# Kernel tuning notes

Measured on AMD Instinct MI355X. Metric: run time of the kernel, lower is better.

Reference implementation:

```python
import jax, jax.numpy as jnp
import numpy as np

INPUT_SIZE = 64
HIDDEN = 128
BATCH = 512
SEQ = 512


def setup_inputs() -> dict:
    key = jax.random.key(0)
    ks = jax.random.split(key, 7)
    s_ih = 1.0 / np.sqrt(HIDDEN)
    token = jax.random.normal(ks[0], (BATCH, SEQ, INPUT_SIZE), dtype=jnp.float32)
    W_ih = jax.random.uniform(ks[1], (HIDDEN, INPUT_SIZE), jnp.float32, -s_ih, s_ih)
    W_hh = jax.random.uniform(ks[2], (HIDDEN, HIDDEN), jnp.float32, -s_ih, s_ih)
    b_ih = jax.random.uniform(ks[3], (HIDDEN,), jnp.float32, -s_ih, s_ih)
    b_hh = jax.random.uniform(ks[4], (HIDDEN,), jnp.float32, -s_ih, s_ih)
    W_lin = jax.random.uniform(ks[5], (1, HIDDEN), jnp.float32, -s_ih, s_ih)
    b_lin = jax.random.uniform(ks[6], (1,), jnp.float32, -s_ih, s_ih)
    return {"token": token, "W_ih": W_ih, "W_hh": W_hh, "b_ih": b_ih,
            "b_hh": b_hh, "W_lin": W_lin, "b_lin": b_lin}


def reference(token, W_ih, W_hh, b_ih, b_hh, W_lin, b_lin):
    # Precompute input projection for all timesteps: [T, B, H]
    x_proj = jnp.einsum('bti,hi->tbh', token, W_ih) + b_ih + b_hh
    h0 = jnp.zeros((token.shape[0], W_hh.shape[0]), dtype=token.dtype)

    def step(h, xp):
        h_new = jnp.tanh(xp + h @ W_hh.T)
        return h_new, None

    h_last, _ = jax.lax.scan(step, h0, x_proj)
    # Linear head on last hidden state: [B, 1]
    return h_last @ W_lin.T + b_lin
```

## Files before the change

### kernel.cpp

```cpp
#include <hip/hip_runtime.h>

#define B_ 512
#define T_ 512
#define I_ 64
#define H_ 128
#define CHUNK 64
#define NCHUNK (T_ / CHUNK)

typedef float4 f4;

__device__ __forceinline__ float fast_tanh(float x) {
    float e = __expf(2.0f * x);
    return 1.0f - 2.0f * __builtin_amdgcn_rcpf(e + 1.0f);
}

template <int CTRL, int BANK>
__device__ __forceinline__ float dppf(float x) {
    return __int_as_float(__builtin_amdgcn_update_dpp(
        0, __float_as_int(x), CTRL, 0xF, BANK, true));
}

__device__ __forceinline__ void gload_lds16(const float* g, float* l) {
    __builtin_amdgcn_global_load_lds(
        (const __attribute__((address_space(1))) unsigned int*)g,
        (__attribute__((address_space(3))) unsigned int*)l, 16, 0, 0);
}

#define FMA4(A, X, W)                      \
    A.x = fmaf((X).x, (W).x, A.x);         \
    A.y = fmaf((X).y, (W).y, A.y);         \
    A.z = fmaf((X).z, (W).z, A.z);         \
    A.w = fmaf((X).w, (W).w, A.w);

#define PIN4(v) asm volatile("" : "+v"((v).x), "+v"((v).y), "+v"((v).z), "+v"((v).w))

__global__ __launch_bounds__(512) __attribute__((amdgpu_waves_per_eu(4, 4)))
void rnn_kernel(const float* __restrict__ token,
                const float* __restrict__ W_ih,
                const float* __restrict__ W_hh,
                const float* __restrict__ b_ih,
                const float* __restrict__ b_hh,
                const float* __restrict__ W_lin,
                const float* __restrict__ b_lin,
                float* __restrict__ out)
{
    __shared__ f4 tok_l[2][CHUNK * 16];
    __shared__ f4 h_l[2][32];

    const int tid = threadIdx.x;
    const int l   = tid & 63;
    const int e   = l & 7;
    const int G   = tid >> 3;
    const int b   = blockIdx.x;

    f4 wh0[4], wh1[4], wi0[2], wi1[2];
    {
        const f4* r0 = (const f4*)(W_hh + (2 * G) * H_ + e * 16);
        const f4* r1 = (const f4*)(W_hh + (2 * G + 1) * H_ + e * 16);
#pragma unroll
        for (int m = 0; m < 4; ++m) { wh0[m] = r0[m]; wh1[m] = r1[m]; }
        const f4* i0 = (const f4*)(W_ih + (2 * G) * I_ + e * 8);
        const f4* i1 = (const f4*)(W_ih + (2 * G + 1) * I_ + e * 8);
#pragma unroll
        for (int m = 0; m < 2; ++m) { wi0[m] = i0[m]; wi1[m] = i1[m]; }
#pragma unroll
        for (int m = 0; m < 4; ++m) { PIN4(wh0[m]); PIN4(wh1[m]); }
        PIN4(wi0[0]); PIN4(wi0[1]); PIN4(wi1[0]); PIN4(wi1[1]);
    }
    const int   jsel    = 2 * G + (e & 1);
    const float my_bias = b_ih[jsel] + b_hh[jsel];
    const int   wloc    = ((jsel >> 2) & 3) * 32 + (jsel >> 4) * 4 + (jsel & 3);
    const bool  writer  = (e < 2);

    const float* tok_row = token + (size_t)b * T_ * I_;

#pragma unroll
    for (int it = 0; it < 2; ++it) {
        const int S = it * 512 + tid;
        const int tt = S >> 4, k = S & 15, m2 = k >> 3, ek = k & 7;
        gload_lds16(tok_row + tt * 64 + ek * 8 + m2 * 4, (float*)&tok_l[0][S]);
    }
    if (tid < H_) ((float*)h_l[0])[tid] = 0.0f;
    asm volatile("s_waitcnt vmcnt(0) lgkmcnt(0)" ::: "memory");
    __builtin_amdgcn_s_barrier();

    f4 t4[2];
    t4[0] = tok_l[0][e];
    t4[1] = tok_l[0][8 + e];

    auto STEP = [&](const f4* hrd, float* hwr, int tt, bool last_in_chunk,
                    bool has_next_chunk, int cb) {
        f4 A0 = {0.f, 0.f, 0.f, 0.f}, A1 = {0.f, 0.f, 0.f, 0.f};
        FMA4(A0, t4[0], wi0[0]);  FMA4(A1, t4[0], wi1[0]);
        FMA4(A0, t4[1], wi0[1]);  FMA4(A1, t4[1], wi1[1]);
#pragma unroll
        for (int m = 0; m < 4; ++m) {
            f4 hv = hrd[m * 8 + e];
            FMA4(A0, hv, wh0[m]);
            FMA4(A1, hv, wh1[m]);
        }
        float p0 = (A0.x + A0.y) + (A0.z + A0.w);
        float p1 = (A1.x + A1.y) + (A1.z + A1.w);
        p0 += dppf<0xB1, 0xF>(p0);
        p1 += dppf<0xB1, 0xF>(p1);
        float c = (e & 1) ? p1 : p0;
        c += dppf<0x4E, 0xF>(c);
        float d1 = dppf<0x104, 0x5>(c);
        float d2 = dppf<0x114, 0xA>(c);
        c = c + d1 + d2;
        float hn = fast_tanh(c + my_bias);
        if (writer) hwr[wloc] = hn;

        if (!last_in_chunk) {
            __builtin_amdgcn_sched_barrier(0);
            t4[0] = tok_l[cb][(tt + 1) * 16 + e];
            t4[1] = tok_l[cb][(tt + 1) * 16 + 8 + e];
            __builtin_amdgcn_sched_barrier(0);
            asm volatile("s_waitcnt lgkmcnt(2)" ::: "memory");
            __builtin_amdgcn_s_barrier();
        } else {
            asm volatile("s_waitcnt vmcnt(0) lgkmcnt(0)" ::: "memory");
            __builtin_amdgcn_s_barrier();
            if (has_next_chunk) {
                t4[0] = tok_l[cb ^ 1][e];
                t4[1] = tok_l[cb ^ 1][8 + e];
            }
        }
    };

#pragma unroll 1
    for (int c = 0; c < NCHUNK; ++c) {
        const int cb = c & 1;
        const bool has_next = (c + 1 < NCHUNK);
        if (has_next) {
            const float* g = tok_row + (size_t)(c + 1) * CHUNK * I_;
#pragma unroll
            for (int it = 0; it < 2; ++it) {
                const int S = it * 512 + tid;
                const int tt = S >> 4, k = S & 15, m2 = k >> 3, ek = k & 7;
                gload_lds16(g + tt * 64 + ek * 8 + m2 * 4, (float*)&tok_l[cb ^ 1][S]);
            }
        }
#pragma unroll 1
        for (int tt = 0; tt < CHUNK; tt += 2) {
            STEP((const f4*)h_l[0], (float*)h_l[1], tt, false, has_next, cb);
            STEP((const f4*)h_l[1], (float*)h_l[0], tt + 1, (tt + 1 == CHUNK - 1),
                 has_next, cb);
        }
    }

    if (tid < 64) {
        const int j0 = tid, j1 = tid + 64;
        const int l0 = ((j0 >> 2) & 3) * 32 + (j0 >> 4) * 4 + (j0 & 3);
        const int l1 = ((j1 >> 2) & 3) * 32 + (j1 >> 4) * 4 + (j1 & 3);
        float p = ((const float*)h_l[0])[l0] * W_lin[j0]
                + ((const float*)h_l[0])[l1] * W_lin[j1];
#pragma unroll
        for (int off = 32; off; off >>= 1) p += __shfl_down(p, off);
        if (tid == 0) out[b] = p + b_lin[0];
    }
}

extern "C" void kernel_launch(void* const* d_in, const int* in_sizes, int n_in,
                              void* d_out, int out_size, void* d_ws, size_t ws_size,
                              hipStream_t stream) {
    const float* token = (const float*)d_in[0];
    const float* W_ih  = (const float*)d_in[1];
    const float* W_hh  = (const float*)d_in[2];
    const float* b_ih  = (const float*)d_in[3];
    const float* b_hh  = (const float*)d_in[4];
    const float* W_lin = (const float*)d_in[5];
    const float* b_lin = (const float*)d_in[6];
    float* out = (float*)d_out;

    hipLaunchKernelGGL(rnn_kernel, dim3(B_), dim3(512), 0, stream,
                       token, W_ih, W_hh, b_ih, b_hh, W_lin, b_lin, out);
}
```

Before: 234.3 us.

## Fold tanh exponent scale into weights and restructure step loop with inline-asm FMAs

Pre-scales W_hh, W_ih and the bias by 2/ln2 so tanh can use a raw v_exp_f32 without a multiply per step. The per-step loop is rewritten without the lambda or the prefetch of the next token, using byte-offset pointer toggling for the h double buffer and loading token vectors directly each step. Inline-asm v_fmac and a multiply-initialised accumulator replace the zero-init FMA chain. The earlier token-load overlap with the barrier is dropped, so each step now waits on the LDS token reads before the FMAs, which may add latency to the critical path.

```diff
diff --git a/kernel.cpp b/kernel.cpp
--- a/kernel.cpp
+++ b/kernel.cpp
@@ -9,10 +9,7 @@
 
 typedef float4 f4;
 
-__device__ __forceinline__ float fast_tanh(float x) {
-    float e = __expf(2.0f * x);
-    return 1.0f - 2.0f * __builtin_amdgcn_rcpf(e + 1.0f);
-}
+#define K2 2.885390081777927f
 
 template <int CTRL, int BANK>
 __device__ __forceinline__ float dppf(float x) {
@@ -26,13 +23,17 @@
         (__attribute__((address_space(3))) unsigned int*)l, 16, 0, 0);
 }
 
-#define FMA4(A, X, W)                      \
-    A.x = fmaf((X).x, (W).x, A.x);         \
-    A.y = fmaf((X).y, (W).y, A.y);         \
-    A.z = fmaf((X).z, (W).z, A.z);         \
-    A.w = fmaf((X).w, (W).w, A.w);
-
-#define PIN4(v) asm volatile("" : "+v"((v).x), "+v"((v).y), "+v"((v).z), "+v"((v).w))
+#define AFMA(a, x, w) asm("v_fmac_f32 %0, %2, %3" : "=v"(a) : "0"(a), "v"(x), "v"(w))
+#define FMA4A(A, X, W)            \
+    AFMA(A.x, (X).x, (W).x);      \
+    AFMA(A.y, (X).y, (W).y);      \
+    AFMA(A.z, (X).z, (W).z);      \
+    AFMA(A.w, (X).w, (W).w)
+#define MUL4(A, X, W)             \
+    A.x = (X).x * (W).x;          \
+    A.y = (X).y * (W).y;          \
+    A.z = (X).z * (W).z;          \
+    A.w = (X).w * (W).w
 
 __global__ __launch_bounds__(512) __attribute__((amdgpu_waves_per_eu(4, 4)))
 void rnn_kernel(const float* __restrict__ token,
@@ -45,11 +46,10 @@
                 float* __restrict__ out)
 {
     __shared__ f4 tok_l[2][CHUNK * 16];
-    __shared__ f4 h_l[2][32];
+    __shared__ f4 h_l[64];
 
     const int tid = threadIdx.x;
-    const int l   = tid & 63;
-    const int e   = l & 7;
+    const int e   = tid & 7;
     const int G   = tid >> 3;
     const int b   = blockIdx.x;
 
@@ -58,94 +58,93 @@
         const f4* r0 = (const f4*)(W_hh + (2 * G) * H_ + e * 16);
         const f4* r1 = (const f4*)(W_hh + (2 * G + 1) * H_ + e * 16);
 #pragma unroll
-        for (int m = 0; m < 4; ++m) { wh0[m] = r0[m]; wh1[m] = r1[m]; }
+        for (int m = 0; m < 4; ++m) {
+            f4 a = r0[m], c = r1[m];
+            wh0[m].x = a.x * K2; wh0[m].y = a.y * K2; wh0[m].z = a.z * K2; wh0[m].w = a.w * K2;
+            wh1[m].x = c.x * K2; wh1[m].y = c.y * K2; wh1[m].z = c.z * K2; wh1[m].w = c.w * K2;
+        }
         const f4* i0 = (const f4*)(W_ih + (2 * G) * I_ + e * 8);
         const f4* i1 = (const f4*)(W_ih + (2 * G + 1) * I_ + e * 8);
 #pragma unroll
-        for (int m = 0; m < 2; ++m) { wi0[m] = i0[m]; wi1[m] = i1[m]; }
-#pragma unroll
-        for (int m = 0; m < 4; ++m) { PIN4(wh0[m]); PIN4(wh1[m]); }
-        PIN4(wi0[0]); PIN4(wi0[1]); PIN4(wi1[0]); PIN4(wi1[1]);
+        for (int m = 0; m < 2; ++m) {
+            f4 a = i0[m], c = i1[m];
+            wi0[m].x = a.x * K2; wi0[m].y = a.y * K2; wi0[m].z = a.z * K2; wi0[m].w = a.w * K2;
+            wi1[m].x = c.x * K2; wi1[m].y = c.y * K2; wi1[m].z = c.z * K2; wi1[m].w = c.w * K2;
+        }
     }
-    const int   jsel    = 2 * G + (e & 1);
-    const float my_bias = b_ih[jsel] + b_hh[jsel];
-    const int   wloc    = ((jsel >> 2) & 3) * 32 + (jsel >> 4) * 4 + (jsel & 3);
-    const bool  writer  = (e < 2);
+    const int   jsel  = 2 * G + (e & 1);
+    const float bias2 = K2 * (b_ih[jsel] + b_hh[jsel]);
+    const int   wloc  = ((jsel >> 2) & 3) * 32 + (jsel >> 4) * 4 + (jsel & 3);
+    const bool  writer = (e < 2);
 
     const float* tok_row = token + (size_t)b * T_ * I_;
 
-#pragma unroll
-    for (int it = 0; it < 2; ++it) {
-        const int S = it * 512 + tid;
-        const int tt = S >> 4, k = S & 15, m2 = k >> 3, ek = k & 7;
-        gload_lds16(tok_row + tt * 64 + ek * 8 + m2 * 4, (float*)&tok_l[0][S]);
-    }
-    if (tid < H_) ((float*)h_l[0])[tid] = 0.0f;
+    const int S0 = tid, S1 = 512 + tid;
+    const int so0 = (S0 >> 4) * 64 + (S0 & 7) * 8 + ((S0 >> 3) & 1) * 4;
+    const int so1 = (S1 >> 4) * 64 + (S1 & 7) * 8 + ((S1 >> 3) & 1) * 4;
+
+    gload_lds16(tok_row + so0, (float*)&tok_l[0][S0]);
+    gload_lds16(tok_row + so1, (float*)&tok_l[0][S1]);
+    if (tid < H_) ((float*)h_l)[tid] = 0.0f;
     asm volatile("s_waitcnt vmcnt(0) lgkmcnt(0)" ::: "memory");
-    __builtin_amdgcn_s_barrier();
+    asm volatile("s_barrier" ::: "memory");
 
-    f4 t4[2];
-    t4[0] = tok_l[0][e];
-    t4[1] = tok_l[0][8 + e];
-
-    auto STEP = [&](const f4* hrd, float* hwr, int tt, bool last_in_chunk,
-                    bool has_next_chunk, int cb) {
-        f4 A0 = {0.f, 0.f, 0.f, 0.f}, A1 = {0.f, 0.f, 0.f, 0.f};
-        FMA4(A0, t4[0], wi0[0]);  FMA4(A1, t4[0], wi1[0]);
-        FMA4(A0, t4[1], wi0[1]);  FMA4(A1, t4[1], wi1[1]);
-#pragma unroll
-        for (int m = 0; m < 4; ++m) {
-            f4 hv = hrd[m * 8 + e];
-            FMA4(A0, hv, wh0[m]);
-            FMA4(A1, hv, wh1[m]);
-        }
-        float p0 = (A0.x + A0.y) + (A0.z + A0.w);
-        float p1 = (A1.x + A1.y) + (A1.z + A1.w);
-        p0 += dppf<0xB1, 0xF>(p0);
-        p1 += dppf<0xB1, 0xF>(p1);
-        float c = (e & 1) ? p1 : p0;
-        c += dppf<0x4E, 0xF>(c);
-        float d1 = dppf<0x104, 0x5>(c);
-        float d2 = dppf<0x114, 0xA>(c);
-        c = c + d1 + d2;
-        float hn = fast_tanh(c + my_bias);
-        if (writer) hwr[wloc] = hn;
-
-        if (!last_in_chunk) {
-            __builtin_amdgcn_sched_barrier(0);
-            t4[0] = tok_l[cb][(tt + 1) * 16 + e];
-            t4[1] = tok_l[cb][(tt + 1) * 16 + 8 + e];
-            __builtin_amdgcn_sched_barrier(0);
-            asm volatile("s_waitcnt lgkmcnt(2)" ::: "memory");
-            __builtin_amdgcn_s_barrier();
-        } else {
-            asm volatile("s_waitcnt vmcnt(0) lgkmcnt(0)" ::: "memory");
-            __builtin_amdgcn_s_barrier();
-            if (has_next_chunk) {
-                t4[0] = tok_l[cb ^ 1][e];
-                t4[1] = tok_l[cb ^ 1][8 + e];
-            }
-        }
-    };
+    const char* hbase = (const char*)h_l;
+    const char* tbase = (const char*)tok_l;
+    unsigned roff = 0;
 
 #pragma unroll 1
     for (int c = 0; c < NCHUNK; ++c) {
         const int cb = c & 1;
-        const bool has_next = (c + 1 < NCHUNK);
-        if (has_next) {
+        if (c + 1 < NCHUNK) {
             const float* g = tok_row + (size_t)(c + 1) * CHUNK * I_;
-#pragma unroll
-            for (int it = 0; it < 2; ++it) {
-                const int S = it * 512 + tid;
-                const int tt = S >> 4, k = S & 15, m2 = k >> 3, ek = k & 7;
-                gload_lds16(g + tt * 64 + ek * 8 + m2 * 4, (float*)&tok_l[cb ^ 1][S]);
-            }
+            float* dst = (float*)(tbase + (cb ^ 1) * (CHUNK * 16 * 16));
+            gload_lds16(g + so0, dst + S0 * 4);
+            gload_lds16(g + so1, dst + S1 * 4);
         }
+        unsigned toff = (unsigned)cb * (CHUNK * 16 * 16);
+
 #pragma unroll 1
-        for (int tt = 0; tt < CHUNK; tt += 2) {
-            STEP((const f4*)h_l[0], (float*)h_l[1], tt, false, has_next, cb);
-            STEP((const f4*)h_l[1], (float*)h_l[0], tt + 1, (tt + 1 == CHUNK - 1),
-                 has_next, cb);
+        for (int tt = 0; tt < CHUNK; ++tt) {
+            const f4* tv  = (const f4*)(tbase + toff);
+            const f4* hrd = (const f4*)(hbase + roff);
+            f4 t0 = tv[e],       t1 = tv[8 + e];
+            f4 h0 = hrd[e],      h1 = hrd[8 + e];
+            f4 h2 = hrd[16 + e], h3 = hrd[24 + e];
+
+            f4 A0, A1;
+            MUL4(A0, t0, wi0[0]);  MUL4(A1, t0, wi1[0]);
+            FMA4A(A0, t1, wi0[1]); FMA4A(A1, t1, wi1[1]);
+            FMA4A(A0, h0, wh0[0]); FMA4A(A1, h0, wh1[0]);
+            FMA4A(A0, h1, wh0[1]); FMA4A(A1, h1, wh1[1]);
+            FMA4A(A0, h2, wh0[2]); FMA4A(A1, h2, wh1[2]);
+            FMA4A(A0, h3, wh0[3]); FMA4A(A1, h3, wh1[3]);
+
+            float p0 = (A0.x + A0.y) + (A0.z + A0.w);
+            float p1 = (A1.x + A1.y) + (A1.z + A1.w);
+            p0 += dppf<0xB1, 0xF>(p0);
+            p1 += dppf<0xB1, 0xF>(p1);
+            float cc = (e & 1) ? p1 : p0;
+            cc += dppf<0x4E, 0xF>(cc);
+            float d1 = dppf<0x104, 0x5>(cc);
+            float d2 = dppf<0x114, 0xA>(cc);
+            cc = cc + d1 + d2;
+            float ex;
+            asm("v_exp_f32 %0, %1" : "=v"(ex) : "v"(cc + bias2));
+            float r = __builtin_amdgcn_rcpf(ex + 1.0f);
+            float hn = 1.0f - (r + r);
+
+            float* hwr = (float*)(hbase + (roff ^ 512));
+            if (writer) hwr[wloc] = hn;
+            asm volatile("s_waitcnt lgkmcnt(0)" ::: "memory");
+            asm volatile("s_barrier" ::: "memory");
+            roff ^= 512;
+            toff += 16 * 16;
+        }
+
+        if (c + 1 < NCHUNK) {
+            asm volatile("s_waitcnt vmcnt(0)" ::: "memory");
+            asm volatile("s_barrier" ::: "memory");
         }
     }
 
@@ -153,8 +152,8 @@
         const int j0 = tid, j1 = tid + 64;
         const int l0 = ((j0 >> 2) & 3) * 32 + (j0 >> 4) * 4 + (j0 & 3);
         const int l1 = ((j1 >> 2) & 3) * 32 + (j1 >> 4) * 4 + (j1 & 3);
-        float p = ((const float*)h_l[0])[l0] * W_lin[j0]
-                + ((const float*)h_l[0])[l1] * W_lin[j1];
+        float p = ((const float*)h_l)[l0] * W_lin[j0]
+                + ((const float*)h_l)[l1] * W_lin[j1];
 #pragma unroll
         for (int off = 32; off; off >>= 1) p += __shfl_down(p, off);
         if (tid == 0) out[b] = p + b_lin[0];
```

Measured after the change: 260.3 us. 1.11x slower.
